# Optimization experiments

Hardware: AMD Instinct MI355X
Metric: run time of the kernel (lower is better)

The kernel has to match this reference:

```python
import jax, jax.numpy as jnp
import numpy as np

N_NODES = 50000
N_EDGES = 800000
N_GRAPHS = 128
INPUT_DIM = 64
HIDDEN = 64       # num_heads * dim_per_head = 4 * 16
N_HEADS = 4
DK = HIDDEN // N_HEADS   # 16, per-head key/query dim
DV = HIDDEN // N_HEADS   # 16, per-head value dim
NUM_LAYERS = 4           # -> 3 GIN layers
OUT_DIM = 16
LN_EPS = 1e-5


def layer_norm(x, g, b):
    mu = jnp.mean(x, axis=-1, keepdims=True)
    var = jnp.mean(jnp.square(x - mu), axis=-1, keepdims=True)
    return (x - mu) * jax.lax.rsqrt(var + LN_EPS) * g + b


def sab_block(x, Wq, Wk, Wv, Wo, ln_g, ln_b, add_residual):
    # x: [N, S, D_in]; pre-LN self-attention block (Set Transformer SAB)
    xin = layer_norm(x, ln_g, ln_b)
    q = jnp.einsum('nsd,dhk->nshk', xin, Wq)   # [N,S,H,dk]
    k = jnp.einsum('nsd,dhk->nshk', xin, Wk)
    v = jnp.einsum('nsd,dhk->nshk', xin, Wv)   # [N,S,H,dv]
    scores = jnp.einsum('nqhk,nshk->nhqs', q, k) / jnp.sqrt(jnp.asarray(DK, x.dtype))
    att = jax.nn.softmax(scores, axis=-1)
    o = jnp.einsum('nhqs,nshk->nqhk', att, v)
    o = o.reshape(o.shape[0], o.shape[1], N_HEADS * DV)
    o = o @ Wo                                  # [N,S,dim_out]
    if add_residual:
        o = o + x
    return o


def gin_aggregate(h, src, dst):
    # sum-neighbor aggregation; eps=0, learn_eps=False -> (1+0)*h + sum_nbrs
    msg = jax.ops.segment_sum(h[src], dst, num_segments=N_NODES)
    return h + msg


def setup_inputs() -> dict:
    key = jax.random.key(0)
    ks = jax.random.split(key, 16)
    s = 0.05
    feat = jax.random.normal(ks[0], (N_NODES, 4 * INPUT_DIM), dtype=jnp.float32)
    src = jax.random.randint(ks[1], (N_EDGES,), 0, N_NODES)
    dst = jax.random.randint(ks[2], (N_EDGES,), 0, N_NODES)
    graph_ids = jnp.sort(jax.random.randint(ks[3], (N_NODES,), 0, N_GRAPHS))
    L = NUM_LAYERS - 1  # 3 GIN layers, all same shapes (input_dim == hidden)
    Wq = jax.random.normal(ks[4], (L, HIDDEN, N_HEADS, DK), dtype=jnp.float32) * s
    Wk = jax.random.normal(ks[5], (L, HIDDEN, N_HEADS, DK), dtype=jnp.float32) * s
    Wv = jax.random.normal(ks[6], (L, HIDDEN, N_HEADS, DV), dtype=jnp.float32) * s
    Wo = jax.random.normal(ks[7], (L, N_HEADS * DV, HIDDEN), dtype=jnp.float32) * s
    sab_ln_g = jnp.ones((L, HIDDEN), dtype=jnp.float32)
    sab_ln_b = jnp.zeros((L, HIDDEN), dtype=jnp.float32)
    ln1_g = jnp.ones((L, HIDDEN), dtype=jnp.float32)
    ln1_b = jnp.zeros((L, HIDDEN), dtype=jnp.float32)
    ln2_g = jnp.ones((L, HIDDEN), dtype=jnp.float32)
    ln2_b = jnp.zeros((L, HIDDEN), dtype=jnp.float32)
    W_pred = jax.random.normal(ks[8], (NUM_LAYERS, HIDDEN, OUT_DIM), dtype=jnp.float32) * s
    b_pred = jnp.zeros((NUM_LAYERS, OUT_DIM), dtype=jnp.float32)
    return {"feat": feat, "src": src, "dst": dst, "graph_ids": graph_ids,
            "Wq": Wq, "Wk": Wk, "Wv": Wv, "Wo": Wo,
            "sab_ln_g": sab_ln_g, "sab_ln_b": sab_ln_b,
            "ln1_g": ln1_g, "ln1_b": ln1_b, "ln2_g": ln2_g, "ln2_b": ln2_b,
            "W_pred": W_pred, "b_pred": b_pred}


def reference(feat, src, dst, graph_ids, Wq, Wk, Wv, Wo,
              sab_ln_g, sab_ln_b, ln1_g, ln1_b, ln2_g, ln2_b, W_pred, b_pred):
    h = feat.reshape(N_NODES, -1, INPUT_DIM)   # [N, S, D]
    hidden_rep = [h]
    for i in range(NUM_LAYERS - 1):
        if i == 0:
            agg = gin_aggregate(h, src, dst)
            h = sab_block(agg, Wq[i], Wk[i], Wv[i], Wo[i],
                          sab_ln_g[i], sab_ln_b[i], add_residual=False)
        else:
            h_pre = layer_norm(h, ln1_g[i], ln1_b[i])
            agg = gin_aggregate(h_pre, src, dst)
            h = h + sab_block(agg, Wq[i], Wk[i], Wv[i], Wo[i],
                              sab_ln_g[i], sab_ln_b[i], add_residual=True)
        hidden_rep.append(layer_norm(jax.nn.relu(h), ln2_g[i], ln2_b[i]))
    score = jnp.zeros((N_GRAPHS, hidden_rep[0].shape[1], OUT_DIM), dtype=feat.dtype)
    for i, hh in enumerate(hidden_rep):
        pooled = jax.ops.segment_sum(hh, graph_ids, num_segments=N_GRAPHS)  # [B,S,D]
        score = score + pooled @ W_pred[i] + b_pred[i]
    return score
```

## Files before the change

kernel.cpp:

```cpp
#include <hip/hip_runtime.h>

#define NN 50000
#define NE 800000
#define NG 128
#define RREP 16
#define RSTRIDE 50048

typedef __attribute__((ext_vector_type(8))) short short8;
typedef __attribute__((ext_vector_type(4))) float f32x4;

__device__ __forceinline__ unsigned short f2bf(float f){
  union { float f; unsigned int u; } v; v.f = f;
  return (unsigned short)((v.u + 0x8000u) >> 16);
}
__device__ __forceinline__ float bf2f(unsigned short h){
  union { unsigned int u; float f; } v; v.u = ((unsigned int)h) << 16;
  return v.f;
}

__global__ __launch_bounds__(256) void k_goff(const int* __restrict__ gid,
                                              int* __restrict__ goff){
  int i = blockIdx.x*256 + threadIdx.x;
  if (i >= NN) return;
  int c = gid[i];
  int p = (i == 0) ? -1 : gid[i-1];
  for (int g = p+1; g <= c; ++g) goff[g] = i;
  if (i == NN-1){
    for (int g = c+1; g <= NG; ++g) goff[g] = NN;
  }
}

__global__ __launch_bounds__(256) void k_count_rep(const int* __restrict__ idx,
                                                   int* __restrict__ cnt_rep, int n){
  int i = blockIdx.x*256 + threadIdx.x;
  int r = blockIdx.x & (RREP-1);
  if (i < n) atomicAdd(&cnt_rep[r*RSTRIDE + idx[i]], 1);
}

__global__ __launch_bounds__(256) void k_reduce_rep(const int* __restrict__ cnt_rep,
                                                    int* __restrict__ cnt){
  int i = blockIdx.x*256 + threadIdx.x;
  if (i < NN){
    int s = 0;
    #pragma unroll
    for (int r=0; r<RREP; ++r) s += cnt_rep[r*RSTRIDE + i];
    cnt[i] = s;
  }
}

__global__ __launch_bounds__(256) void k_blocksum(const int* __restrict__ in, int n,
                                                  int* __restrict__ bsum){
  __shared__ int ws4[4];
  int i = blockIdx.x*256 + threadIdx.x;
  int v = (i < n) ? in[i] : 0;
  #pragma unroll
  for (int d=1; d<64; d<<=1) v += __shfl_xor(v, d);
  int lane = threadIdx.x & 63, w = threadIdx.x >> 6;
  if (lane == 0) ws4[w] = v;
  __syncthreads();
  if (threadIdx.x == 0) bsum[blockIdx.x] = ws4[0]+ws4[1]+ws4[2]+ws4[3];
}

__global__ __launch_bounds__(256) void k_scan_small(const int* __restrict__ in, int n,
                                                    int* __restrict__ out){
  __shared__ int wsum[4];
  int tid = threadIdx.x, lane = tid & 63, w = tid >> 6;
  int v = (tid < n) ? in[tid] : 0;
  int x = v;
  #pragma unroll
  for (int d=1; d<64; d<<=1){ int y = __shfl_up(x, d); if (lane >= d) x += y; }
  if (lane == 63) wsum[w] = x;
  __syncthreads();
  int pre2 = 0;
  for (int j=0; j<w; ++j) pre2 += wsum[j];
  int incl = x + pre2;
  if (tid < n) out[tid] = incl - v;
  if (tid == n-1) out[n] = incl;
}

__global__ __launch_bounds__(256) void k_scan_apply(const int* __restrict__ in, int n,
                                                    const int* __restrict__ boff,
                                                    int* __restrict__ out){
  __shared__ int wsum[4];
  int tid = threadIdx.x, lane = tid & 63, w = tid >> 6;
  int i = blockIdx.x*256 + tid;
  int v = (i < n) ? in[i] : 0;
  int x = v;
  #pragma unroll
  for (int d=1; d<64; d<<=1){ int y = __shfl_up(x, d); if (lane >= d) x += y; }
  if (lane == 63) wsum[w] = x;
  __syncthreads();
  int pre2 = boff[blockIdx.x];
  for (int j=0; j<w; ++j) pre2 += wsum[j];
  int excl = x - v + pre2;
  if (i < n){
    out[i] = excl;
    if (i == n-1) out[n] = excl + v;
  }
}

__global__ __launch_bounds__(256) void k_fpos_rep(const int* __restrict__ cnt_rep,
                                                  const int* __restrict__ off,
                                                  int* __restrict__ fpos_rep){
  int i = blockIdx.x*256 + threadIdx.x;
  if (i < NN){
    int p = off[i];
    #pragma unroll
    for (int r=0; r<RREP; ++r){
      fpos_rep[r*RSTRIDE + i] = p;
      p += cnt_rep[r*RSTRIDE + i];
    }
  }
}

__global__ __launch_bounds__(256) void k_fill_rep(const int* __restrict__ src,
                                                  const int* __restrict__ dst,
                                                  int* __restrict__ fpos_rep,
                                                  int* __restrict__ csr, int n){
  int i = blockIdx.x*256 + threadIdx.x;
  int r = blockIdx.x & (RREP-1);
  if (i < n){
    int p = atomicAdd(&fpos_rep[r*RSTRIDE + dst[i]], 1);
    csr[p] = src[i];
  }
}

__global__ __launch_bounds__(256) void k_wt(const float* __restrict__ Wq,
                                            const float* __restrict__ Wk,
                                            const float* __restrict__ Wv,
                                            const float* __restrict__ Wo,
                                            unsigned short* __restrict__ Wt){
  int gid = blockIdx.x*256 + threadIdx.x;
  int l   = gid >> 14;
  int rem = gid & 16383;
  int mat = rem >> 12;
  int idx = rem & 4095;
  int c = idx >> 6, n = idx & 63;
  const float* srcp = (mat==0)?Wq:(mat==1)?Wk:(mat==2)?Wv:Wo;
  float v = srcp[l*4096 + idx];
  Wt[l*16384 + (mat*64 + n)*64 + c] = f2bf(v);
}

__global__ __launch_bounds__(256) void k_f2bf_c(const float* __restrict__ in,
                                                unsigned short* __restrict__ out){
  int i = blockIdx.x*256 + threadIdx.x;
  float4 v = ((const float4*)in)[i];
  ushort4 o; o.x=f2bf(v.x); o.y=f2bf(v.y); o.z=f2bf(v.z); o.w=f2bf(v.w);
  int flat = i << 2;
  int node = flat >> 8, f = flat & 255;
  int chunk = f >> 5;
  ((ushort4*)out)[(size_t)chunk*NN*8 + node*8 + ((f & 31) >> 2)] = o;
}

__global__ __launch_bounds__(256) void k_agg_x(const unsigned short* __restrict__ pre_c,
                                               const int* __restrict__ off,
                                               const int* __restrict__ csr,
                                               unsigned short* __restrict__ agg){
  int chunk = blockIdx.x & 7;
  int seg   = blockIdx.x >> 3;
  int w = threadIdx.x >> 6, lane = threadIdx.x & 63;
  int lg = lane >> 3, li = lane & 7;
  int node = seg*32 + w*8 + lg;
  if (node >= NN) return;
  const ushort4* slice = (const ushort4*)pre_c + (size_t)chunk*NN*8;
  int s = off[node], e = off[node+1];
  ushort4 u = slice[node*8 + li];
  float a0 = bf2f(u.x), a1 = bf2f(u.y), a2 = bf2f(u.z), a3 = bf2f(u.w);
  int i = s;
  for (; i + 2 <= e; i += 2){
    int n0 = csr[i], n1 = csr[i+1];
    ushort4 u0 = slice[n0*8 + li], u1 = slice[n1*8 + li];
    a0 += bf2f(u0.x)+bf2f(u1.x);
    a1 += bf2f(u0.y)+bf2f(u1.y);
    a2 += bf2f(u0.z)+bf2f(u1.z);
    a3 += bf2f(u0.w)+bf2f(u1.w);
  }
  if (i < e){
    int n0 = csr[i];
    ushort4 u0 = slice[n0*8 + li];
    a0 += bf2f(u0.x); a1 += bf2f(u0.y); a2 += bf2f(u0.z); a3 += bf2f(u0.w);
  }
  ushort4 o; o.x=f2bf(a0); o.y=f2bf(a1); o.z=f2bf(a2); o.w=f2bf(a3);
  ((ushort4*)agg)[node*64 + chunk*8 + li] = o;
}

__global__ __launch_bounds__(256) void k_sab(const unsigned short* __restrict__ agg,
                                             unsigned short* __restrict__ h,
                                             unsigned short* __restrict__ lnout,
                                             unsigned short* __restrict__ pre_next,
                                             const unsigned short* __restrict__ Wt,
                                             const float* __restrict__ lng,
                                             const float* __restrict__ lnb,
                                             const float* __restrict__ g2,
                                             const float* __restrict__ b2,
                                             const float* __restrict__ g1,
                                             const float* __restrict__ b1,
                                             int residual, int write_pre, int write_h){
  __shared__ unsigned short xo_s[4][16][72];
  __shared__ unsigned short agg_s[4][16][72];
  __shared__ unsigned short qkv_s[4][16][200];

  int tid = threadIdx.x;
  int w = tid >> 6, lane = tid & 63;
  int c16 = lane & 15, kb = lane >> 4;
  int R0 = blockIdx.x*64 + w*16;

  {
    float4 gv = ((const float4*)lng)[c16];
    float4 bv = ((const float4*)lnb)[c16];
    #pragma unroll
    for (int rr=0; rr<4; ++rr){
      int m = rr*4 + kb;
      ushort4 uv = ((const ushort4*)agg)[(R0+m)*16 + c16];
      if (residual) *(ushort4*)&agg_s[w][m][c16*4] = uv;
      float vx = bf2f(uv.x), vy = bf2f(uv.y), vz = bf2f(uv.z), vw = bf2f(uv.w);
      float s = vx+vy+vz+vw;
      float q = vx*vx+vy*vy+vz*vz+vw*vw;
      #pragma unroll
      for (int d=1; d<16; d<<=1){ s += __shfl_xor(s, d); q += __shfl_xor(q, d); }
      float mu = s*(1.f/64.f);
      float rs = rsqrtf(q*(1.f/64.f) - mu*mu + 1e-5f);
      ushort4 o;
      o.x=f2bf((vx-mu)*rs*gv.x+bv.x); o.y=f2bf((vy-mu)*rs*gv.y+bv.y);
      o.z=f2bf((vz-mu)*rs*gv.z+bv.z); o.w=f2bf((vw-mu)*rs*gv.w+bv.w);
      *(ushort4*)&xo_s[w][m][c16*4] = o;
    }
  }

  short8 a0v = *(const short8*)&xo_s[w][c16][kb*8];
  short8 a1v = *(const short8*)&xo_s[w][c16][32 + kb*8];
  f32x4 acc[12];
  #pragma unroll
  for (int t=0; t<12; ++t){
    short8 b0 = *(const short8*)&Wt[(t*16 + c16)*64 + kb*8];
    short8 b1 = *(const short8*)&Wt[(t*16 + c16)*64 + 32 + kb*8];
    f32x4 z = {0.f, 0.f, 0.f, 0.f};
    z = __builtin_amdgcn_mfma_f32_16x16x32_bf16(a0v, b0, z, 0, 0, 0);
    z = __builtin_amdgcn_mfma_f32_16x16x32_bf16(a1v, b1, z, 0, 0, 0);
    acc[t] = z;
  }
  #pragma unroll
  for (int t=0; t<12; ++t){
    #pragma unroll
    for (int r=0; r<4; ++r)
      qkv_s[w][kb*4 + r][t*16 + c16] = f2bf(acc[t][r]);
  }

  {
    int p = lane >> 2, qr = lane & 3;
    int ns = p >> 2, hd = p & 3;
    int mrow = ns*4 + qr;
    int qc = hd*16, kc = 64 + hd*16, vc = 128 + hd*16;
    float qv[16];
    short8 u0 = *(const short8*)&qkv_s[w][mrow][qc];
    short8 u1 = *(const short8*)&qkv_s[w][mrow][qc+8];
    #pragma unroll
    for (int j=0; j<8; ++j){
      qv[j]   = bf2f((unsigned short)u0[j]);
      qv[8+j] = bf2f((unsigned short)u1[j]);
    }
    float sc[4];
    #pragma unroll
    for (int kr=0; kr<4; ++kr){
      short8 k0 = *(const short8*)&qkv_s[w][ns*4+kr][kc];
      short8 k1 = *(const short8*)&qkv_s[w][ns*4+kr][kc+8];
      float d2 = 0.f;
      #pragma unroll
      for (int j=0; j<8; ++j){
        d2 += qv[j]  *bf2f((unsigned short)k0[j]);
        d2 += qv[8+j]*bf2f((unsigned short)k1[j]);
      }
      sc[kr] = d2 * 0.25f;
    }
    float mx = fmaxf(fmaxf(sc[0],sc[1]), fmaxf(sc[2],sc[3]));
    float e0=__expf(sc[0]-mx), e1=__expf(sc[1]-mx), e2=__expf(sc[2]-mx), e3=__expf(sc[3]-mx);
    float inv = 1.f/(e0+e1+e2+e3);
    float at[4] = {e0*inv, e1*inv, e2*inv, e3*inv};
    float ov[16];
    #pragma unroll
    for (int j=0; j<16; ++j) ov[j] = 0.f;
    #pragma unroll
    for (int kr=0; kr<4; ++kr){
      short8 v0 = *(const short8*)&qkv_s[w][ns*4+kr][vc];
      short8 v1 = *(const short8*)&qkv_s[w][ns*4+kr][vc+8];
      #pragma unroll
      for (int j=0; j<8; ++j){
        ov[j]   += at[kr]*bf2f((unsigned short)v0[j]);
        ov[8+j] += at[kr]*bf2f((unsigned short)v1[j]);
      }
    }
    short8 s0v, s1v;
    #pragma unroll
    for (int j=0; j<8; ++j){
      s0v[j] = (short)f2bf(ov[j]);
      s1v[j] = (short)f2bf(ov[8+j]);
    }
    *(short8*)&xo_s[w][mrow][qc]   = s0v;
    *(short8*)&xo_s[w][mrow][qc+8] = s1v;
  }

  {
    short8 oa0 = *(const short8*)&xo_s[w][c16][kb*8];
    short8 oa1 = *(const short8*)&xo_s[w][c16][32 + kb*8];
    #pragma unroll
    for (int t=0; t<4; ++t){
      short8 b0 = *(const short8*)&Wt[(192 + t*16 + c16)*64 + kb*8];
      short8 b1 = *(const short8*)&Wt[(192 + t*16 + c16)*64 + 32 + kb*8];
      f32x4 z = {0.f, 0.f, 0.f, 0.f};
      z = __builtin_amdgcn_mfma_f32_16x16x32_bf16(oa0, b0, z, 0, 0, 0);
      z = __builtin_amdgcn_mfma_f32_16x16x32_bf16(oa1, b1, z, 0, 0, 0);
      #pragma unroll
      for (int r=0; r<4; ++r)
        xo_s[w][kb*4 + r][t*16 + c16] = f2bf(z[r]);
    }
  }

  float4 g2v = ((const float4*)g2)[c16];
  float4 b2v = ((const float4*)b2)[c16];
  float4 g1v, b1v;
  if (write_pre){ g1v = ((const float4*)g1)[c16]; b1v = ((const float4*)b1)[c16]; }
  #pragma unroll
  for (int rr=0; rr<4; ++rr){
    int m = rr*4 + kb;
    int row = R0 + m;
    ushort4 uv = *(const ushort4*)&xo_s[w][m][c16*4];
    float v0 = bf2f(uv.x), v1 = bf2f(uv.y), v2 = bf2f(uv.z), v3 = bf2f(uv.w);
    if (residual){
      ushort4 hh = ((const ushort4*)h)[row*16 + c16];
      ushort4 ag = *(const ushort4*)&agg_s[w][m][c16*4];
      v0 += bf2f(hh.x) + bf2f(ag.x);
      v1 += bf2f(hh.y) + bf2f(ag.y);
      v2 += bf2f(hh.z) + bf2f(ag.z);
      v3 += bf2f(hh.w) + bf2f(ag.w);
    }
    float r0 = fmaxf(v0,0.f), r1 = fmaxf(v1,0.f), r2 = fmaxf(v2,0.f), r3 = fmaxf(v3,0.f);
    float s1 = v0+v1+v2+v3, q1 = v0*v0+v1*v1+v2*v2+v3*v3;
    float s2 = r0+r1+r2+r3, q2 = r0*r0+r1*r1+r2*r2+r3*r3;
    #pragma unroll
    for (int d=1; d<16; d<<=1){
      s1 += __shfl_xor(s1, d); q1 += __shfl_xor(q1, d);
      s2 += __shfl_xor(s2, d); q2 += __shfl_xor(q2, d);
    }
    float mu1 = s1*(1.f/64.f), rs1 = rsqrtf(q1*(1.f/64.f) - mu1*mu1 + 1e-5f);
    float mu2 = s2*(1.f/64.f), rs2 = rsqrtf(q2*(1.f/64.f) - mu2*mu2 + 1e-5f);
    if (write_h){
      ushort4 o; o.x=f2bf(v0); o.y=f2bf(v1); o.z=f2bf(v2); o.w=f2bf(v3);
      ((ushort4*)h)[row*16 + c16] = o;
    }
    {
      ushort4 o;
      o.x=f2bf((r0-mu2)*rs2*g2v.x+b2v.x); o.y=f2bf((r1-mu2)*rs2*g2v.y+b2v.y);
      o.z=f2bf((r2-mu2)*rs2*g2v.z+b2v.z); o.w=f2bf((r3-mu2)*rs2*g2v.w+b2v.w);
      ((ushort4*)lnout)[row*16 + c16] = o;
    }
    if (write_pre){
      int nd = row >> 2;
      int f = (row & 3)*64 + 4*c16;
      int chunk = f >> 5;
      ushort4 o;
      o.x=f2bf((v0-mu1)*rs1*g1v.x+b1v.x); o.y=f2bf((v1-mu1)*rs1*g1v.y+b1v.y);
      o.z=f2bf((v2-mu1)*rs1*g1v.z+b1v.z); o.w=f2bf((v3-mu1)*rs1*g1v.w+b1v.w);
      ((ushort4*)pre_next)[(size_t)chunk*NN*8 + nd*8 + ((f & 31) >> 2)] = o;
    }
  }
}

__global__ __launch_bounds__(256) void k_pool8(const float* __restrict__ src,
                                               const int* __restrict__ goff,
                                               float* __restrict__ out){
  int g = blockIdx.x >> 3, sub = blockIdx.x & 7, t = threadIdx.x;
  int s = goff[g], e = goff[g+1], len = e - s;
  int s0 = s + ((len*sub) >> 3), e0 = s + ((len*(sub+1)) >> 3);
  float a0=0.f, a1=0.f;
  int n = s0;
  for (; n + 2 <= e0; n += 2){ a0 += src[n*256 + t]; a1 += src[(n+1)*256 + t]; }
  if (n < e0) a0 += src[n*256 + t];
  atomicAdd(&out[g*256 + t], a0 + a1);
}

__global__ __launch_bounds__(256) void k_pool8b(const unsigned short* __restrict__ src,
                                                const int* __restrict__ goff,
                                                float* __restrict__ out){
  int g = blockIdx.x >> 3, sub = blockIdx.x & 7, t = threadIdx.x;
  int s = goff[g], e = goff[g+1], len = e - s;
  int s0 = s + ((len*sub) >> 3), e0 = s + ((len*(sub+1)) >> 3);
  float a0=0.f, a1=0.f;
  int n = s0;
  for (; n + 2 <= e0; n += 2){ a0 += bf2f(src[n*256 + t]); a1 += bf2f(src[(n+1)*256 + t]); }
  if (n < e0) a0 += bf2f(src[n*256 + t]);
  atomicAdd(&out[g*256 + t], a0 + a1);
}

__global__ __launch_bounds__(256) void k_final(const float* __restrict__ pooled,
                                               const float* __restrict__ Wp,
                                               const float* __restrict__ bp,
                                               float* __restrict__ out){
  int t = blockIdx.x*256 + threadIdx.x;
  int b = t >> 6, s = (t >> 4) & 3, o = t & 15;
  float acc = 0.f;
  for (int i=0; i<4; ++i){
    acc += bp[i*16 + o];
    const float* pr = pooled + i*32768 + b*256 + s*64;
    const float* wp = Wp + i*1024 + o;
    float a = 0.f;
    #pragma unroll 8
    for (int c=0; c<64; ++c) a += pr[c]*wp[c*16];
    acc += a;
  }
  out[t] = acc;
}

static const size_t OFF_H     = 0;
static const size_t OFF_LNOUT = 25600000;
static const size_t OFF_PRE0  = 51200000;
static const size_t OFF_PRE1  = 76800000;
static const size_t OFF_AGG   = 102400000;
static const size_t OFF_CSR   = 128000000;
static const size_t OFF_CNT   = 131200000;
static const size_t OFF_OFF   = 131400064;
static const size_t OFF_GOFF  = 131600128;
static const size_t OFF_POOL  = 131600704;
static const size_t OFF_WT    = 132124992;
static const size_t OFF_BSUM  = 132223296;
static const size_t OFF_BOFF  = 132224128;

extern "C" void kernel_launch(void* const* d_in, const int* in_sizes, int n_in,
                              void* d_out, int out_size, void* d_ws, size_t ws_size,
                              hipStream_t stream) {
  const float* feat = (const float*)d_in[0];
  const int*   src  = (const int*)d_in[1];
  const int*   dst  = (const int*)d_in[2];
  const int*   gid  = (const int*)d_in[3];
  const float* Wq   = (const float*)d_in[4];
  const float* Wk   = (const float*)d_in[5];
  const float* Wv   = (const float*)d_in[6];
  const float* Wo   = (const float*)d_in[7];
  const float* sg   = (const float*)d_in[8];
  const float* sb   = (const float*)d_in[9];
  const float* l1g  = (const float*)d_in[10];
  const float* l1b  = (const float*)d_in[11];
  const float* l2g  = (const float*)d_in[12];
  const float* l2b  = (const float*)d_in[13];
  const float* Wp   = (const float*)d_in[14];
  const float* bp   = (const float*)d_in[15];
  float* out = (float*)d_out;

  char* ws = (char*)d_ws;
  unsigned short* h      = (unsigned short*)(ws + OFF_H);
  unsigned short* lnout  = (unsigned short*)(ws + OFF_LNOUT);
  unsigned short* pre0   = (unsigned short*)(ws + OFF_PRE0);
  unsigned short* pre1   = (unsigned short*)(ws + OFF_PRE1);
  unsigned short* agg    = (unsigned short*)(ws + OFF_AGG);
  int*            csr    = (int*)(ws + OFF_CSR);
  int*            cnt    = (int*)(ws + OFF_CNT);
  int*            off    = (int*)(ws + OFF_OFF);
  int*            goff   = (int*)(ws + OFF_GOFF);
  float*          pooled = (float*)(ws + OFF_POOL);
  unsigned short* Wt     = (unsigned short*)(ws + OFF_WT);
  int*            bsum   = (int*)(ws + OFF_BSUM);
  int*            boff   = (int*)(ws + OFF_BOFF);
  int*            cnt_rep  = (int*)(ws + OFF_H);
  int*            fpos_rep = (int*)(ws + OFF_H + (size_t)RREP*RSTRIDE*4);

  hipMemsetAsync(cnt_rep, 0, (size_t)RREP*RSTRIDE*4, stream);
  hipMemsetAsync(pooled, 0, 4*NG*256*sizeof(float), stream);

  k_count_rep<<<NE/256, 256, 0, stream>>>(dst, cnt_rep, NE);
  k_goff<<<(NN+255)/256, 256, 0, stream>>>(gid, goff);
  k_reduce_rep<<<(NN+255)/256, 256, 0, stream>>>(cnt_rep, cnt);
  k_blocksum<<<196, 256, 0, stream>>>(cnt, NN, bsum);
  k_scan_small<<<1, 256, 0, stream>>>(bsum, 196, boff);
  k_scan_apply<<<196, 256, 0, stream>>>(cnt, NN, boff, off);
  k_fpos_rep<<<(NN+255)/256, 256, 0, stream>>>(cnt_rep, off, fpos_rep);
  k_fill_rep<<<NE/256, 256, 0, stream>>>(src, dst, fpos_rep, csr, NE);

  k_wt<<<192, 256, 0, stream>>>(Wq, Wk, Wv, Wo, Wt);
  k_f2bf_c<<<12500, 256, 0, stream>>>(feat, pre0);
  k_pool8<<<NG*8, 256, 0, stream>>>(feat, goff, pooled + 0*32768);

  int aggBlocks = 1563*8;

  k_agg_x<<<aggBlocks, 256, 0, stream>>>(pre0, off, csr, agg);
  k_sab<<<3125, 256, 0, stream>>>(agg, h, lnout, pre1, Wt + 0*16384,
                                  sg + 0, sb + 0, l2g + 0, l2b + 0,
                                  l1g + 1*64, l1b + 1*64, 0, 1, 1);
  k_pool8b<<<NG*8, 256, 0, stream>>>(lnout, goff, pooled + 1*32768);

  k_agg_x<<<aggBlocks, 256, 0, stream>>>(pre1, off, csr, agg);
  k_sab<<<3125, 256, 0, stream>>>(agg, h, lnout, pre0, Wt + 1*16384,
                                  sg + 1*64, sb + 1*64, l2g + 1*64, l2b + 1*64,
                                  l1g + 2*64, l1b + 2*64, 1, 1, 1);
  k_pool8b<<<NG*8, 256, 0, stream>>>(lnout, goff, pooled + 2*32768);

  k_agg_x<<<aggBlocks, 256, 0, stream>>>(pre0, off, csr, agg);
  k_sab<<<3125, 256, 0, stream>>>(agg, h, lnout, pre1, Wt + 2*16384,
                                  sg + 2*64, sb + 2*64, l2g + 2*64, l2b + 2*64,
                                  l1g + 2*64, l1b + 2*64, 1, 0, 0);
  k_pool8b<<<NG*8, 256, 0, stream>>>(lnout, goff, pooled + 3*32768);

  k_final<<<32, 256, 0, stream>>>(pooled, Wp, bp, out);
}
```

Baseline: 667.0 us.

## Compute SAB attention directly from MFMA accumulator registers, dropping qkv shared staging

The small 4x4 per-head attention is now computed straight from the MFMA output fragments. Score dot products are reduced across the 16 head-dim lanes with xor shuffles instead of writing q/k/v to LDS and re-reading them. The residual agg values are also kept in registers rather than in a second shared buffer. This removes a large LDS round trip and its bf16 rounding and lowers LDS usage, which may raise occupancy. In exchange it adds many cross-lane shuffles (16 values times 4 steps per head), drops the max-subtraction in the softmax, and increases register pressure.

Measured after the change: 726.4 us. 8.9% more time.

```diff
diff --git a/kernel.cpp b/kernel.cpp
--- a/kernel.cpp
+++ b/kernel.cpp
@@ -197,14 +197,13 @@
                                              const float* __restrict__ b1,
                                              int residual, int write_pre, int write_h){
   __shared__ unsigned short xo_s[4][16][72];
-  __shared__ unsigned short agg_s[4][16][72];
-  __shared__ unsigned short qkv_s[4][16][200];
 
   int tid = threadIdx.x;
   int w = tid >> 6, lane = tid & 63;
   int c16 = lane & 15, kb = lane >> 4;
   int R0 = blockIdx.x*64 + w*16;
 
+  ushort4 av[4];
   {
     float4 gv = ((const float4*)lng)[c16];
     float4 bv = ((const float4*)lnb)[c16];
@@ -212,7 +211,7 @@
     for (int rr=0; rr<4; ++rr){
       int m = rr*4 + kb;
       ushort4 uv = ((const ushort4*)agg)[(R0+m)*16 + c16];
-      if (residual) *(ushort4*)&agg_s[w][m][c16*4] = uv;
+      av[rr] = uv;
       float vx = bf2f(uv.x), vy = bf2f(uv.y), vz = bf2f(uv.z), vw = bf2f(uv.w);
       float s = vx+vy+vz+vw;
       float q = vx*vx+vy*vy+vz*vz+vw*vw;
@@ -239,64 +238,30 @@
     z = __builtin_amdgcn_mfma_f32_16x16x32_bf16(a1v, b1, z, 0, 0, 0);
     acc[t] = z;
   }
-  #pragma unroll
-  for (int t=0; t<12; ++t){
-    #pragma unroll
-    for (int r=0; r<4; ++r)
-      qkv_s[w][kb*4 + r][t*16 + c16] = f2bf(acc[t][r]);
-  }
-
-  {
-    int p = lane >> 2, qr = lane & 3;
-    int ns = p >> 2, hd = p & 3;
-    int mrow = ns*4 + qr;
-    int qc = hd*16, kc = 64 + hd*16, vc = 128 + hd*16;
-    float qv[16];
-    short8 u0 = *(const short8*)&qkv_s[w][mrow][qc];
-    short8 u1 = *(const short8*)&qkv_s[w][mrow][qc+8];
-    #pragma unroll
-    for (int j=0; j<8; ++j){
-      qv[j]   = bf2f((unsigned short)u0[j]);
-      qv[8+j] = bf2f((unsigned short)u1[j]);
-    }
-    float sc[4];
-    #pragma unroll
-    for (int kr=0; kr<4; ++kr){
-      short8 k0 = *(const short8*)&qkv_s[w][ns*4+kr][kc];
-      short8 k1 = *(const short8*)&qkv_s[w][ns*4+kr][kc+8];
-      float d2 = 0.f;
+
+  #pragma unroll
+  for (int hd=0; hd<4; ++hd){
+    float sc[4][4];
+    #pragma unroll
+    for (int s1=0; s1<4; ++s1)
       #pragma unroll
-      for (int j=0; j<8; ++j){
-        d2 += qv[j]  *bf2f((unsigned short)k0[j]);
-        d2 += qv[8+j]*bf2f((unsigned short)k1[j]);
-      }
-      sc[kr] = d2 * 0.25f;
-    }
-    float mx = fmaxf(fmaxf(sc[0],sc[1]), fmaxf(sc[2],sc[3]));
-    float e0=__expf(sc[0]-mx), e1=__expf(sc[1]-mx), e2=__expf(sc[2]-mx), e3=__expf(sc[3]-mx);
-    float inv = 1.f/(e0+e1+e2+e3);
-    float at[4] = {e0*inv, e1*inv, e2*inv, e3*inv};
-    float ov[16];
-    #pragma unroll
-    for (int j=0; j<16; ++j) ov[j] = 0.f;
-    #pragma unroll
-    for (int kr=0; kr<4; ++kr){
-      short8 v0 = *(const short8*)&qkv_s[w][ns*4+kr][vc];
-      short8 v1 = *(const short8*)&qkv_s[w][ns*4+kr][vc+8];
+      for (int s2=0; s2<4; ++s2)
+        sc[s1][s2] = acc[hd][s1]*acc[4+hd][s2];
+    #pragma unroll
+    for (int d=1; d<16; d<<=1)
       #pragma unroll
-      for (int j=0; j<8; ++j){
-        ov[j]   += at[kr]*bf2f((unsigned short)v0[j]);
-        ov[8+j] += at[kr]*bf2f((unsigned short)v1[j]);
-      }
-    }
-    short8 s0v, s1v;
-    #pragma unroll
-    for (int j=0; j<8; ++j){
-      s0v[j] = (short)f2bf(ov[j]);
-      s1v[j] = (short)f2bf(ov[8+j]);
-    }
-    *(short8*)&xo_s[w][mrow][qc]   = s0v;
-    *(short8*)&xo_s[w][mrow][qc+8] = s1v;
+      for (int s1=0; s1<4; ++s1)
+        #pragma unroll
+        for (int s2=0; s2<4; ++s2)
+          sc[s1][s2] += __shfl_xor(sc[s1][s2], d);
+    #pragma unroll
+    for (int s1=0; s1<4; ++s1){
+      float e0 = __expf(sc[s1][0]*0.25f), e1 = __expf(sc[s1][1]*0.25f);
+      float e2 = __expf(sc[s1][2]*0.25f), e3 = __expf(sc[s1][3]*0.25f);
+      float inv = 1.f/(e0+e1+e2+e3);
+      float o = (e0*acc[8+hd][0] + e1*acc[8+hd][1] + e2*acc[8+hd][2] + e3*acc[8+hd][3])*inv;
+      xo_s[w][kb*4 + s1][hd*16 + c16] = f2bf(o);
+    }
   }
 
   {
@@ -327,11 +292,10 @@
     float v0 = bf2f(uv.x), v1 = bf2f(uv.y), v2 = bf2f(uv.z), v3 = bf2f(uv.w);
     if (residual){
       ushort4 hh = ((const ushort4*)h)[row*16 + c16];
-      ushort4 ag = *(const ushort4*)&agg_s[w][m][c16*4];
-      v0 += bf2f(hh.x) + bf2f(ag.x);
-      v1 += bf2f(hh.y) + bf2f(ag.y);
-      v2 += bf2f(hh.z) + bf2f(ag.z);
-      v3 += bf2f(hh.w) + bf2f(ag.w);
+      v0 += bf2f(hh.x) + bf2f(av[rr].x);
+      v1 += bf2f(hh.y) + bf2f(av[rr].y);
+      v2 += bf2f(hh.z) + bf2f(av[rr].z);
+      v3 += bf2f(hh.w) + bf2f(av[rr].w);
     }
     float r0 = fmaxf(v0,0.f), r1 = fmaxf(v1,0.f), r2 = fmaxf(v2,0.f), r3 = fmaxf(v3,0.f);
     float s1 = v0+v1+v2+v3, q1 = v0*v0+v1*v1+v2*v2+v3*v3;
```

## Fuse graph pooling into SAB epilogue via run-length atomics; keep agg in registers

Applied to the files above, without the earlier changes.

The graph-level sum pooling of the post-ReLU layer-norm output moves into the SAB kernel's epilogue. Each thread accumulates its 4 rows (one node) per graph id and issues float atomics only when the graph changes. This removes the lnout bf16 write and read plus three separate pooling launches. The aggregated input is also held in registers instead of a shared-memory copy for the residual, which cuts LDS use. The cost is many more global atomics (about 4 per thread per block) contending on the same 128x256 pooled buffer, and a change in float summation order.

New measurement: 742.9 us. 1.11x slower.

```diff
diff --git a/kernel.cpp b/kernel.cpp
--- a/kernel.cpp
+++ b/kernel.cpp
@@ -186,9 +186,10 @@
 
 __global__ __launch_bounds__(256) void k_sab(const unsigned short* __restrict__ agg,
                                              unsigned short* __restrict__ h,
-                                             unsigned short* __restrict__ lnout,
                                              unsigned short* __restrict__ pre_next,
                                              const unsigned short* __restrict__ Wt,
+                                             const int* __restrict__ gid,
+                                             float* __restrict__ pooled,
                                              const float* __restrict__ lng,
                                              const float* __restrict__ lnb,
                                              const float* __restrict__ g2,
@@ -197,7 +198,6 @@
                                              const float* __restrict__ b1,
                                              int residual, int write_pre, int write_h){
   __shared__ unsigned short xo_s[4][16][72];
-  __shared__ unsigned short agg_s[4][16][72];
   __shared__ unsigned short qkv_s[4][16][200];
 
   int tid = threadIdx.x;
@@ -205,6 +205,7 @@
   int c16 = lane & 15, kb = lane >> 4;
   int R0 = blockIdx.x*64 + w*16;
 
+  ushort4 av[4];
   {
     float4 gv = ((const float4*)lng)[c16];
     float4 bv = ((const float4*)lnb)[c16];
@@ -212,7 +213,7 @@
     for (int rr=0; rr<4; ++rr){
       int m = rr*4 + kb;
       ushort4 uv = ((const ushort4*)agg)[(R0+m)*16 + c16];
-      if (residual) *(ushort4*)&agg_s[w][m][c16*4] = uv;
+      av[rr] = uv;
       float vx = bf2f(uv.x), vy = bf2f(uv.y), vz = bf2f(uv.z), vw = bf2f(uv.w);
       float s = vx+vy+vz+vw;
       float q = vx*vx+vy*vy+vz*vz+vw*vw;
@@ -319,6 +320,9 @@
   float4 b2v = ((const float4*)b2)[c16];
   float4 g1v, b1v;
   if (write_pre){ g1v = ((const float4*)g1)[c16]; b1v = ((const float4*)b1)[c16]; }
+  float p0=0.f, p1=0.f, p2=0.f, p3=0.f;
+  int gcur = -1;
+  int pbase = kb*64 + c16*4;
   #pragma unroll
   for (int rr=0; rr<4; ++rr){
     int m = rr*4 + kb;
@@ -327,11 +331,10 @@
     float v0 = bf2f(uv.x), v1 = bf2f(uv.y), v2 = bf2f(uv.z), v3 = bf2f(uv.w);
     if (residual){
       ushort4 hh = ((const ushort4*)h)[row*16 + c16];
-      ushort4 ag = *(const ushort4*)&agg_s[w][m][c16*4];
-      v0 += bf2f(hh.x) + bf2f(ag.x);
-      v1 += bf2f(hh.y) + bf2f(ag.y);
-      v2 += bf2f(hh.z) + bf2f(ag.z);
-      v3 += bf2f(hh.w) + bf2f(ag.w);
+      v0 += bf2f(hh.x) + bf2f(av[rr].x);
+      v1 += bf2f(hh.y) + bf2f(av[rr].y);
+      v2 += bf2f(hh.z) + bf2f(av[rr].z);
+      v3 += bf2f(hh.w) + bf2f(av[rr].w);
     }
     float r0 = fmaxf(v0,0.f), r1 = fmaxf(v1,0.f), r2 = fmaxf(v2,0.f), r3 = fmaxf(v3,0.f);
     float s1 = v0+v1+v2+v3, q1 = v0*v0+v1*v1+v2*v2+v3*v3;
@@ -348,10 +351,22 @@
       ((ushort4*)h)[row*16 + c16] = o;
     }
     {
-      ushort4 o;
-      o.x=f2bf((r0-mu2)*rs2*g2v.x+b2v.x); o.y=f2bf((r1-mu2)*rs2*g2v.y+b2v.y);
-      o.z=f2bf((r2-mu2)*rs2*g2v.z+b2v.z); o.w=f2bf((r3-mu2)*rs2*g2v.w+b2v.w);
-      ((ushort4*)lnout)[row*16 + c16] = o;
+      int node = (R0 >> 2) + rr;
+      int g = gid[node];
+      float l0 = (r0-mu2)*rs2*g2v.x+b2v.x;
+      float l1 = (r1-mu2)*rs2*g2v.y+b2v.y;
+      float l2 = (r2-mu2)*rs2*g2v.z+b2v.z;
+      float l3 = (r3-mu2)*rs2*g2v.w+b2v.w;
+      if (g != gcur){
+        if (gcur >= 0){
+          float* pp = pooled + gcur*256 + pbase;
+          atomicAdd(pp+0, p0); atomicAdd(pp+1, p1);
+          atomicAdd(pp+2, p2); atomicAdd(pp+3, p3);
+        }
+        gcur = g; p0 = l0; p1 = l1; p2 = l2; p3 = l3;
+      } else {
+        p0 += l0; p1 += l1; p2 += l2; p3 += l3;
+      }
     }
     if (write_pre){
       int nd = row >> 2;
@@ -362,6 +377,11 @@
       o.z=f2bf((v2-mu1)*rs1*g1v.z+b1v.z); o.w=f2bf((v3-mu1)*rs1*g1v.w+b1v.w);
       ((ushort4*)pre_next)[(size_t)chunk*NN*8 + nd*8 + ((f & 31) >> 2)] = o;
     }
+  }
+  {
+    float* pp = pooled + gcur*256 + pbase;
+    atomicAdd(pp+0, p0); atomicAdd(pp+1, p1);
+    atomicAdd(pp+2, p2); atomicAdd(pp+3, p3);
   }
 }
 
@@ -375,19 +395,6 @@
   int n = s0;
   for (; n + 2 <= e0; n += 2){ a0 += src[n*256 + t]; a1 += src[(n+1)*256 + t]; }
   if (n < e0) a0 += src[n*256 + t];
-  atomicAdd(&out[g*256 + t], a0 + a1);
-}
-
-__global__ __launch_bounds__(256) void k_pool8b(const unsigned short* __restrict__ src,
-                                                const int* __restrict__ goff,
-                                                float* __restrict__ out){
-  int g = blockIdx.x >> 3, sub = blockIdx.x & 7, t = threadIdx.x;
-  int s = goff[g], e = goff[g+1], len = e - s;
-  int s0 = s + ((len*sub) >> 3), e0 = s + ((len*(sub+1)) >> 3);
-  float a0=0.f, a1=0.f;
-  int n = s0;
-  for (; n + 2 <= e0; n += 2){ a0 += bf2f(src[n*256 + t]); a1 += bf2f(src[(n+1)*256 + t]); }
-  if (n < e0) a0 += bf2f(src[n*256 + t]);
   atomicAdd(&out[g*256 + t], a0 + a1);
 }
 
@@ -411,7 +418,6 @@
 }
 
 static const size_t OFF_H     = 0;
-static const size_t OFF_LNOUT = 25600000;
 static const size_t OFF_PRE0  = 51200000;
 static const size_t OFF_PRE1  = 76800000;
 static const size_t OFF_AGG   = 102400000;
@@ -447,7 +453,6 @@
 
   char* ws = (char*)d_ws;
   unsigned short* h      = (unsigned short*)(ws + OFF_H);
-  unsigned short* lnout  = (unsigned short*)(ws + OFF_LNOUT);
   unsigned short* pre0   = (unsigned short*)(ws + OFF_PRE0);
   unsigned short* pre1   = (unsigned short*)(ws + OFF_PRE1);
   unsigned short* agg    = (unsigned short*)(ws + OFF_AGG);
@@ -481,22 +486,19 @@
   int aggBlocks = 1563*8;
 
   k_agg_x<<<aggBlocks, 256, 0, stream>>>(pre0, off, csr, agg);
-  k_sab<<<3125, 256, 0, stream>>>(agg, h, lnout, pre1, Wt + 0*16384,
+  k_sab<<<3125, 256, 0, stream>>>(agg, h, pre1, Wt + 0*16384, gid, pooled + 1*32768,
                                   sg + 0, sb + 0, l2g + 0, l2b + 0,
                                   l1g + 1*64, l1b + 1*64, 0, 1, 1);
-  k_pool8b<<<NG*8, 256, 0, stream>>>(lnout, goff, pooled + 1*32768);
 
   k_agg_x<<<aggBlocks, 256, 0, stream>>>(pre1, off, csr, agg);
-  k_sab<<<3125, 256, 0, stream>>>(agg, h, lnout, pre0, Wt + 1*16384,
+  k_sab<<<3125, 256, 0, stream>>>(agg, h, pre0, Wt + 1*16384, gid, pooled + 2*32768,
                                   sg + 1*64, sb + 1*64, l2g + 1*64, l2b + 1*64,
                                   l1g + 2*64, l1b + 2*64, 1, 1, 1);
-  k_pool8b<<<NG*8, 256, 0, stream>>>(lnout, goff, pooled + 2*32768);
 
   k_agg_x<<<aggBlocks, 256, 0, stream>>>(pre0, off, csr, agg);
-  k_sab<<<3125, 256, 0, stream>>>(agg, h, lnout, pre1, Wt + 2*16384,
+  k_sab<<<3125, 256, 0, stream>>>(agg, h, pre1, Wt + 2*16384, gid, pooled + 3*32768,
                                   sg + 2*64, sb + 2*64, l2g + 2*64, l2b + 2*64,
                                   l1g + 2*64, l1b + 2*64, 1, 0, 0);
-  k_pool8b<<<NG*8, 256, 0, stream>>>(lnout, goff, pooled + 3*32768);
 
   k_final<<<32, 256, 0, stream>>>(pooled, Wp, bp, out);
 }
```
